# Performance work log

Measured on AMD Instinct MI355X. Metric: run time of the kernel, lower is better.

The kernel has to match this reference:

```python
import jax, jax.numpy as jnp
import numpy as np

EPSILON = 1e-07
N = 33554432  # 2^25 elements


def setup_inputs() -> dict:
    key = jax.random.key(0)
    k1, k2 = jax.random.split(key)
    y_pred = jax.random.uniform(k1, (N,), dtype=jnp.float32)
    y_true = jax.random.randint(k2, (N,), 0, 2, dtype=jnp.int64)
    return {"y_pred": y_pred, "y_true": y_true}


def reference(y_pred, y_true):
    # one-hot true labels: [N, 2]
    y_true_oh = jax.nn.one_hot(y_true, 2, dtype=jnp.float32)
    # vectorized equivalent of the per-element loop:
    # if pred < 0.5 -> [pred, 1-pred] else [1-pred, pred]
    col0 = jnp.where(y_pred < 0.5, y_pred, 1.0 - y_pred)
    yp = jnp.stack([col0, 1.0 - col0], axis=1)  # [N, 2]
    tp = jnp.sum(y_true_oh * yp, axis=0)
    tn = jnp.sum((1.0 - y_true_oh) * (1.0 - yp), axis=0)
    fp = jnp.sum((1.0 - y_true_oh) * yp, axis=0)
    fn = jnp.sum(y_true_oh * (1.0 - yp), axis=0)
    precision = tp / (tp + fp + EPSILON)
    recall = tp / (tp + fn + EPSILON)
    f1 = 2.0 * (precision * recall) / (precision + recall + EPSILON)
    f1 = jnp.clip(f1, EPSILON, 1.0 - EPSILON)
    return 1.0 - jnp.mean(f1)
```

## Files before the change

### kernel.cpp

```cpp
#include <hip/hip_runtime.h>

#define EPSILON 1e-7

constexpr int BLOCKS  = 2048;
constexpr int THREADS = 256;

__global__ __launch_bounds__(THREADS) void f1_partial_kernel(
    const float* __restrict__ pred,
    const int*   __restrict__ truth,
    float*       __restrict__ partial,
    int n4)
{
    float s0 = 0.0f, s1 = 0.0f;
    int   c1 = 0;

    const float4* p4 = reinterpret_cast<const float4*>(pred);
    const int4*   t4 = reinterpret_cast<const int4*>(truth);

    int idx    = blockIdx.x * blockDim.x + threadIdx.x;
    int stride = gridDim.x * blockDim.x;

    for (int i = idx; i < n4; i += stride) {
        float4 p = p4[i];
        int4   t = t4[i];
        float c;
        c = (p.x < 0.5f) ? p.x : 1.0f - p.x; if (t.x) s1 += c; else s0 += c; c1 += t.x;
        c = (p.y < 0.5f) ? p.y : 1.0f - p.y; if (t.y) s1 += c; else s0 += c; c1 += t.y;
        c = (p.z < 0.5f) ? p.z : 1.0f - p.z; if (t.z) s1 += c; else s0 += c; c1 += t.z;
        c = (p.w < 0.5f) ? p.w : 1.0f - p.w; if (t.w) s1 += c; else s0 += c; c1 += t.w;
    }

    #pragma unroll
    for (int off = 32; off > 0; off >>= 1) {
        s0 += __shfl_down(s0, off);
        s1 += __shfl_down(s1, off);
        c1 += __shfl_down(c1, off);
    }

    __shared__ float ls0[THREADS / 64];
    __shared__ float ls1[THREADS / 64];
    __shared__ int   lc1[THREADS / 64];

    int lane = threadIdx.x & 63;
    int wave = threadIdx.x >> 6;
    if (lane == 0) { ls0[wave] = s0; ls1[wave] = s1; lc1[wave] = c1; }
    __syncthreads();

    if (threadIdx.x == 0) {
        float t0 = 0.0f, t1 = 0.0f; int tc = 0;
        #pragma unroll
        for (int w = 0; w < THREADS / 64; ++w) { t0 += ls0[w]; t1 += ls1[w]; tc += lc1[w]; }
        partial[3 * blockIdx.x + 0] = t0;
        partial[3 * blockIdx.x + 1] = t1;
        partial[3 * blockIdx.x + 2] = (float)tc;
    }
}

__global__ __launch_bounds__(THREADS) void f1_final_kernel(
    const float* __restrict__ partial,
    float*       __restrict__ out,
    int nblocks, double n_total)
{
    double s0 = 0.0, s1 = 0.0, c1 = 0.0;
    for (int i = threadIdx.x; i < nblocks; i += blockDim.x) {
        s0 += (double)partial[3 * i + 0];
        s1 += (double)partial[3 * i + 1];
        c1 += (double)partial[3 * i + 2];
    }

    #pragma unroll
    for (int off = 32; off > 0; off >>= 1) {
        s0 += __shfl_down(s0, off);
        s1 += __shfl_down(s1, off);
        c1 += __shfl_down(c1, off);
    }

    __shared__ double ds0[THREADS / 64];
    __shared__ double ds1[THREADS / 64];
    __shared__ double dc1[THREADS / 64];

    int lane = threadIdx.x & 63;
    int wave = threadIdx.x >> 6;
    if (lane == 0) { ds0[wave] = s0; ds1[wave] = s1; dc1[wave] = c1; }
    __syncthreads();

    if (threadIdx.x == 0) {
        double S0 = 0.0, S1 = 0.0, C1 = 0.0;
        #pragma unroll
        for (int w = 0; w < THREADS / 64; ++w) { S0 += ds0[w]; S1 += ds1[w]; C1 += dc1[w]; }

        double n1 = C1, n0 = n_total - n1;
        double tp0 = S0,      fp0 = S1,      fn0 = n0 - S0;
        double tp1 = n1 - S1, fp1 = n0 - S0, fn1 = S1;

        double p0 = tp0 / (tp0 + fp0 + EPSILON);
        double r0 = tp0 / (tp0 + fn0 + EPSILON);
        double f0 = 2.0 * p0 * r0 / (p0 + r0 + EPSILON);
        f0 = fmin(fmax(f0, (double)EPSILON), 1.0 - (double)EPSILON);

        double p1 = tp1 / (tp1 + fp1 + EPSILON);
        double r1 = tp1 / (tp1 + fn1 + EPSILON);
        double f1 = 2.0 * p1 * r1 / (p1 + r1 + EPSILON);
        f1 = fmin(fmax(f1, (double)EPSILON), 1.0 - (double)EPSILON);

        out[0] = (float)(1.0 - 0.5 * (f0 + f1));
    }
}

extern "C" void kernel_launch(void* const* d_in, const int* in_sizes, int n_in,
                              void* d_out, int out_size, void* d_ws, size_t ws_size,
                              hipStream_t stream) {
    const float* pred  = (const float*)d_in[0];
    const int*   truth = (const int*)d_in[1];
    float*       out   = (float*)d_out;
    float*       partial = (float*)d_ws;

    int n  = in_sizes[0];
    int n4 = n / 4;

    f1_partial_kernel<<<BLOCKS, THREADS, 0, stream>>>(pred, truth, partial, n4);
    f1_final_kernel<<<1, THREADS, 0, stream>>>(partial, out, BLOCKS, (double)n);
}
```

Measured before the change: 50.03 us.

## Fuse final reduction into single kernel via fixed-point atomics and last-block ticket

Replaces the two-kernel reduction with one pass: each block atomically adds fixed-point scaled partial sums into a global accumulator, and the last block (via ticket counter) computes the F1 loss. This removes the second kernel launch and partial-array round trip, but adds a memset launch and fixed-point quantization of the sums (scale 2^38) that could overflow or lose precision.

```diff
diff --git a/kernel.cpp b/kernel.cpp
--- a/kernel.cpp
+++ b/kernel.cpp
@@ -5,11 +5,21 @@
 constexpr int BLOCKS  = 2048;
 constexpr int THREADS = 256;
 
-__global__ __launch_bounds__(THREADS) void f1_partial_kernel(
+#define FP_SCALE 274877906944.0f
+
+struct Accum {
+    unsigned long long s0;
+    unsigned long long s1;
+    unsigned long long n1;
+    unsigned int       ticket;
+};
+
+__global__ __launch_bounds__(THREADS) void f1_onepass_kernel(
     const float* __restrict__ pred,
     const int*   __restrict__ truth,
-    float*       __restrict__ partial,
-    int n4)
+    Accum*       __restrict__ acc,
+    float*       __restrict__ out,
+    int n4, double n_total)
 {
     float s0 = 0.0f, s1 = 0.0f;
     int   c1 = 0;
@@ -50,60 +60,40 @@
         float t0 = 0.0f, t1 = 0.0f; int tc = 0;
         #pragma unroll
         for (int w = 0; w < THREADS / 64; ++w) { t0 += ls0[w]; t1 += ls1[w]; tc += lc1[w]; }
-        partial[3 * blockIdx.x + 0] = t0;
-        partial[3 * blockIdx.x + 1] = t1;
-        partial[3 * blockIdx.x + 2] = (float)tc;
-    }
-}
 
-__global__ __launch_bounds__(THREADS) void f1_final_kernel(
-    const float* __restrict__ partial,
-    float*       __restrict__ out,
-    int nblocks, double n_total)
-{
-    double s0 = 0.0, s1 = 0.0, c1 = 0.0;
-    for (int i = threadIdx.x; i < nblocks; i += blockDim.x) {
-        s0 += (double)partial[3 * i + 0];
-        s1 += (double)partial[3 * i + 1];
-        c1 += (double)partial[3 * i + 2];
-    }
+        atomicAdd(&acc->s0, (unsigned long long)llrintf(t0 * FP_SCALE));
+        atomicAdd(&acc->s1, (unsigned long long)llrintf(t1 * FP_SCALE));
+        atomicAdd(&acc->n1, (unsigned long long)tc);
 
-    #pragma unroll
-    for (int off = 32; off > 0; off >>= 1) {
-        s0 += __shfl_down(s0, off);
-        s1 += __shfl_down(s1, off);
-        c1 += __shfl_down(c1, off);
-    }
+        __threadfence();
+        unsigned int prev = atomicAdd(&acc->ticket, 1u);
 
-    __shared__ double ds0[THREADS / 64];
-    __shared__ double ds1[THREADS / 64];
-    __shared__ double dc1[THREADS / 64];
+        if (prev == (unsigned int)(BLOCKS - 1)) {
+            __threadfence();
+            unsigned long long us0 = __hip_atomic_load(&acc->s0, __ATOMIC_RELAXED, __HIP_MEMORY_SCOPE_AGENT);
+            unsigned long long us1 = __hip_atomic_load(&acc->s1, __ATOMIC_RELAXED, __HIP_MEMORY_SCOPE_AGENT);
+            unsigned long long un1 = __hip_atomic_load(&acc->n1, __ATOMIC_RELAXED, __HIP_MEMORY_SCOPE_AGENT);
 
-    int lane = threadIdx.x & 63;
-    int wave = threadIdx.x >> 6;
-    if (lane == 0) { ds0[wave] = s0; ds1[wave] = s1; dc1[wave] = c1; }
-    __syncthreads();
+            double S0 = (double)us0 / (double)FP_SCALE;
+            double S1 = (double)us1 / (double)FP_SCALE;
+            double n1 = (double)un1;
+            double n0 = n_total - n1;
 
-    if (threadIdx.x == 0) {
-        double S0 = 0.0, S1 = 0.0, C1 = 0.0;
-        #pragma unroll
-        for (int w = 0; w < THREADS / 64; ++w) { S0 += ds0[w]; S1 += ds1[w]; C1 += dc1[w]; }
+            double tp0 = S0,      fp0 = S1,      fn0 = n0 - S0;
+            double tp1 = n1 - S1, fp1 = n0 - S0, fn1 = S1;
 
-        double n1 = C1, n0 = n_total - n1;
-        double tp0 = S0,      fp0 = S1,      fn0 = n0 - S0;
-        double tp1 = n1 - S1, fp1 = n0 - S0, fn1 = S1;
+            double p0 = tp0 / (tp0 + fp0 + EPSILON);
+            double r0 = tp0 / (tp0 + fn0 + EPSILON);
+            double f0 = 2.0 * p0 * r0 / (p0 + r0 + EPSILON);
+            f0 = fmin(fmax(f0, (double)EPSILON), 1.0 - (double)EPSILON);
 
-        double p0 = tp0 / (tp0 + fp0 + EPSILON);
-        double r0 = tp0 / (tp0 + fn0 + EPSILON);
-        double f0 = 2.0 * p0 * r0 / (p0 + r0 + EPSILON);
-        f0 = fmin(fmax(f0, (double)EPSILON), 1.0 - (double)EPSILON);
+            double p1 = tp1 / (tp1 + fp1 + EPSILON);
+            double r1 = tp1 / (tp1 + fn1 + EPSILON);
+            double f1 = 2.0 * p1 * r1 / (p1 + r1 + EPSILON);
+            f1 = fmin(fmax(f1, (double)EPSILON), 1.0 - (double)EPSILON);
 
-        double p1 = tp1 / (tp1 + fp1 + EPSILON);
-        double r1 = tp1 / (tp1 + fn1 + EPSILON);
-        double f1 = 2.0 * p1 * r1 / (p1 + r1 + EPSILON);
-        f1 = fmin(fmax(f1, (double)EPSILON), 1.0 - (double)EPSILON);
-
-        out[0] = (float)(1.0 - 0.5 * (f0 + f1));
+            out[0] = (float)(1.0 - 0.5 * (f0 + f1));
+        }
     }
 }
 
@@ -113,11 +103,13 @@
     const float* pred  = (const float*)d_in[0];
     const int*   truth = (const int*)d_in[1];
     float*       out   = (float*)d_out;
-    float*       partial = (float*)d_ws;
+    Accum*       acc   = (Accum*)d_ws;
 
-    int n  = in_sizes[0];
-    int n4 = n / 4;
+    int    n       = in_sizes[0];
+    int    n4      = n / 4;
+    double n_total = (double)n;
 
-    f1_partial_kernel<<<BLOCKS, THREADS, 0, stream>>>(pred, truth, partial, n4);
-    f1_final_kernel<<<1, THREADS, 0, stream>>>(partial, out, BLOCKS, (double)n);
+    hipMemsetAsync(d_ws, 0, sizeof(Accum), stream);
+
+    f1_onepass_kernel<<<BLOCKS, THREADS, 0, stream>>>(pred, truth, acc, out, n4, n_total);
 }
```

Result: slower. 141.9 us (+183.7%).
